# Kernel tuning notes

Measured on AMD Instinct MI355X. Metric: run time of the kernel, lower is better.

The kernel has to match this reference:

```python
import jax, jax.numpy as jnp
import numpy as np

EPS = 1e-6
GROUPS = 32


def group_norm(x, scale, bias):
    # x: [b, c, h, w], GroupNorm(32, c, eps=1e-6, affine=True)
    b, c, h, w = x.shape
    xg = x.reshape(b, GROUPS, c // GROUPS, h, w)
    mean = jnp.mean(xg, axis=(2, 3, 4), keepdims=True)
    var = jnp.var(xg, axis=(2, 3, 4), keepdims=True)
    xg = (xg - mean) * jax.lax.rsqrt(var + EPS)
    x = xg.reshape(b, c, h, w)
    return x * scale[None, :, None, None] + bias[None, :, None, None]


def conv1x1(x, w, b):
    # w: [out_c, in_c], b: [out_c]
    return jnp.einsum('oc,bchw->bohw', w, x) + b[None, :, None, None]


def setup_inputs() -> dict:
    key = jax.random.key(0)
    ks = jax.random.split(key, 12)
    c = 512
    b, h, w = 16, 32, 32
    s = 1.0 / np.sqrt(c)
    return {
        'x': jax.random.normal(ks[0], (b, c, h, w), jnp.float32),
        'y': jax.random.normal(ks[1], (b, c, h, w), jnp.float32),
        'norm_scale': jnp.ones((c,), jnp.float32),
        'norm_bias': jnp.zeros((c,), jnp.float32),
        'norm1_scale': jnp.ones((c,), jnp.float32),
        'norm1_bias': jnp.zeros((c,), jnp.float32),
        'wq': jax.random.normal(ks[2], (c, c), jnp.float32) * s,
        'bq': jnp.zeros((c,), jnp.float32),
        'wk': jax.random.normal(ks[3], (c, c), jnp.float32) * s,
        'bk': jnp.zeros((c,), jnp.float32),
        'wv': jax.random.normal(ks[4], (c, c), jnp.float32) * s,
        'bv': jnp.zeros((c,), jnp.float32),
        'wp': jax.random.normal(ks[5], (c, c), jnp.float32) * s,
        'bp': jnp.zeros((c,), jnp.float32),
    }


def reference(x, y, norm_scale, norm_bias, norm1_scale, norm1_bias,
              wq, bq, wk, bk, wv, bv, wp, bp):
    b, c, h, w = x.shape
    hw = h * w
    h_ = group_norm(x, norm_scale, norm_bias)
    k = conv1x1(h_, wk, bk).reshape(b, c, hw)          # [b, c, hw]
    v = conv1x1(h_, wv, bv).reshape(b, c, hw)          # [b, c, hw]
    y_ = group_norm(y, norm1_scale, norm1_bias)
    q = conv1x1(y_, wq, bq).reshape(b, c, hw)          # [b, c, hw]
    # attn[b, i, j] = sum_c q[b,c,i] * k[b,c,j]
    attn = jnp.einsum('bci,bcj->bij', q, k) * (int(c) ** -0.5)
    attn = jax.nn.softmax(attn, axis=2)
    # out[b, c, i] = sum_j v[b,c,j] * attn[b,i,j]
    out = jnp.einsum('bcj,bij->bci', v, attn).reshape(b, c, h, w)
    out = conv1x1(out, wp, bp)
    return x + out
```

## Files before the change

kernel.cpp:

```cpp
#include <hip/hip_runtime.h>
#include <hip/hip_bf16.h>

typedef __bf16 bf16;
typedef __bf16 bf16x8 __attribute__((ext_vector_type(8)));
typedef __bf16 bf16x4 __attribute__((ext_vector_type(4)));
typedef float f32x4 __attribute__((ext_vector_type(4)));
typedef unsigned short u16;
typedef unsigned short u16x8 __attribute__((ext_vector_type(8)));

constexpr int kHW = 1024;
constexpr int kC  = 512;

__device__ inline float wave_sum(float v) {
#pragma unroll
    for (int o = 32; o; o >>= 1) v += __shfl_xor(v, o, 64);
    return v;
}

__device__ inline float b2f(u16 u) {
    union { float f; unsigned i; } z; z.i = ((unsigned)u) << 16; return z.f;
}

__device__ inline void gload_lds16(const void* g, void* l) {
    __builtin_amdgcn_global_load_lds(
        (const __attribute__((address_space(1))) void*)g,
        (__attribute__((address_space(3))) void*)l, 16, 0, 0);
}

#define VMCNT(n) asm volatile("s_waitcnt vmcnt(" #n ")" ::: "memory")
#define SBAR __builtin_amdgcn_s_barrier()
#define NOP do {} while (0)

__global__ __launch_bounds__(256) void gn2w_kernel(
    const float* __restrict__ x0, const float* __restrict__ s0,
    const float* __restrict__ b0, bf16* __restrict__ o0,
    const float* __restrict__ x1, const float* __restrict__ s1,
    const float* __restrict__ b1, bf16* __restrict__ o1,
    const float* __restrict__ wq, const float* __restrict__ wk,
    const float* __restrict__ wv, const float* __restrict__ wp,
    const float* __restrict__ bq, const float* __restrict__ bk,
    const float* __restrict__ bv, const float* __restrict__ bp,
    bf16* __restrict__ wdst, float* __restrict__ bpk)
{
    int bid = blockIdx.x;
    int t = threadIdx.x;
    if (bid >= 1024) {
        int i = (bid - 1024) * 256 + t;
        wdst[i]            = (bf16)wq[i];
        wdst[262144 + i]   = (bf16)wk[i];
        wdst[2*262144 + i] = (bf16)wv[i];
        wdst[3*262144 + i] = (bf16)wp[i];
        if (i < 2048) {
            int j = i >> 9, c = i & 511;
            const float* s = j == 0 ? bq : j == 1 ? bk : j == 2 ? bv : bp;
            bpk[i] = s[c];
        }
        return;
    }

    __shared__ u16 xs[16][1032];
    __shared__ float red[8];
    __shared__ float ab[2][16];

    int xcd = bid & 7, idx = bid >> 3;
    int pair = xcd * 4 + (idx >> 5);
    int g = idx & 31;
    int sel = pair >> 4;
    int b = pair & 15;

    const float* x = sel ? x1 : x0;
    const float* scale = sel ? s1 : s0;
    const float* bias  = sel ? b1 : b0;
    bf16* outT = sel ? o1 : o0;

    int c0 = g * 16;
    const float* xg = x + ((size_t)b * kC + c0) * kHW;

    float s = 0.f, s2 = 0.f;
    const float4* xg4 = reinterpret_cast<const float4*>(xg);
#pragma unroll
    for (int i = 0; i < 16; ++i) {
        float4 v = xg4[t + i * 256];
        bf16x4 r;
        r[0] = (bf16)v.x; r[1] = (bf16)v.y; r[2] = (bf16)v.z; r[3] = (bf16)v.w;
        *reinterpret_cast<bf16x4*>(&xs[i][t * 4]) = r;
        s  += v.x + v.y + v.z + v.w;
        s2 += v.x*v.x + v.y*v.y + v.z*v.z + v.w*v.w;
    }
    s = wave_sum(s); s2 = wave_sum(s2);
    int lane = t & 63, wid = t >> 6;
    if (!lane) { red[wid] = s; red[4 + wid] = s2; }
    __syncthreads();
    float ts = red[0] + red[1] + red[2] + red[3];
    float t2 = red[4] + red[5] + red[6] + red[7];
    float mean = ts * (1.f / 16384.f);
    float var  = t2 * (1.f / 16384.f) - mean * mean;
    float inv  = rsqrtf(var + 1e-6f);

    if (t < 16) {
        float a = inv * scale[c0 + t];
        ab[0][t] = a;
        ab[1][t] = bias[c0 + t] - mean * a;
    }
    __syncthreads();

    int cg = t & 3, spw = t >> 2;
    float a0 = ab[0][cg*4],   a1 = ab[0][cg*4+1],
          a2 = ab[0][cg*4+2], a3 = ab[0][cg*4+3];
    float d0 = ab[1][cg*4],   d1 = ab[1][cg*4+1],
          d2 = ab[1][cg*4+2], d3 = ab[1][cg*4+3];
    bf16* ob = outT + (size_t)b * kHW * kC + c0 + cg * 4;
#pragma unroll
    for (int i = 0; i < 16; ++i) {
        int sp = spw + i * 64;
        bf16x4 w;
        w[0] = (bf16)(b2f(xs[cg*4 + 0][sp]) * a0 + d0);
        w[1] = (bf16)(b2f(xs[cg*4 + 1][sp]) * a1 + d1);
        w[2] = (bf16)(b2f(xs[cg*4 + 2][sp]) * a2 + d2);
        w[3] = (bf16)(b2f(xs[cg*4 + 3][sp]) * a3 + d3);
        *reinterpret_cast<bf16x4*>(ob + (size_t)sp * kC) = w;
    }
}

template <int BIAS, bool RESID, typename OUT_T, bool STATS, int NBX, int NBY>
__global__ __launch_bounds__(512, 2) void gemm256(
    const bf16* __restrict__ Ab, size_t sA, int lda,
    const bf16* __restrict__ Bb, size_t sB, int ldb,
    OUT_T* __restrict__ Cb, size_t sC, int ldc,
    const float* __restrict__ biasB, int sBias,
    const float* __restrict__ residB, size_t sR,
    float alpha, float* __restrict__ statsOut)
{
    __shared__ u16 lds[65536];
    constexpr int NT = 8;

    int bid = blockIdx.x, nwg = gridDim.x;
    int swz = (bid & 7) * (nwg >> 3) + (bid >> 3);
    int job = swz / (NBX * NBY), rem = swz % (NBX * NBY);
    int by = rem / NBX, bx = rem % NBX;
    int brow = by * 256, bcol = bx * 256;

    const u16* Au = reinterpret_cast<const u16*>(Ab + (size_t)job * sA);
    const u16* Bu = reinterpret_cast<const u16*>(Bb + (size_t)job * sB);

    int t = threadIdx.x;
    int lane = t & 63, w = t >> 6;
    int wm = w >> 2, wn = w & 3;
    int cc = lane & 15, nib = lane >> 4;

    int trow = t >> 3;
    int gsrc = ((t & 7) ^ (trow & 7)) * 8;
    const u16* Asrc = Au + (size_t)(brow + trow) * lda + gsrc;
    const u16* Bsrc = Bu + (size_t)(bcol + trow) * ldb + gsrc;
    u16* LDSA = lds;
    u16* LDSB = lds + 32768;

#define STAGE_A(TL, Q) gload_lds16(Asrc + (size_t)(Q) * 64 * lda + (TL) * 64, \
                                   LDSA + (((TL)&1)*4 + (Q)) * 4096 + t * 8)
#define STAGE_B(TL, Q) gload_lds16(Bsrc + (size_t)(Q) * 64 * ldb + (TL) * 64, \
                                   LDSB + (((TL)&1)*4 + (Q)) * 4096 + t * 8)

    f32x4 acc[8][4] = {};
    bf16x8 afr[4][2], bfr[4][2];

#define PHASE(MH, NH, TL, STG, WTC)                                           \
  {                                                                           \
    if ((NH) == 0) {                                                          \
      _Pragma("unroll") for (int mi = 0; mi < 4; ++mi)                        \
      _Pragma("unroll") for (int kx = 0; kx < 2; ++kx)                        \
        afr[mi][kx] = *reinterpret_cast<const bf16x8*>(LDSA +                 \
            (((TL)&1)*4 + wm*2 + (MH)) * 4096 + (mi*16 + cc) * 64 +           \
            (((nib + kx*4) ^ (cc & 7)) * 8));                                 \
    }                                                                         \
    if ((MH) == 0) {                                                          \
      _Pragma("unroll") for (int ni = 0; ni < 2; ++ni)                        \
      _Pragma("unroll") for (int kx = 0; kx < 2; ++kx)                        \
        bfr[(NH)*2 + ni][kx] = *reinterpret_cast<const bf16x8*>(LDSB +        \
            (((TL)&1)*4 + wn) * 4096 + (((NH)*2 + ni)*16 + cc) * 64 +         \
            (((nib + kx*4) ^ (cc & 7)) * 8));                                 \
    }                                                                         \
    STG;                                                                      \
    SBAR;                                                                     \
    __builtin_amdgcn_s_setprio(1);                                            \
    _Pragma("unroll") for (int mi = 0; mi < 4; ++mi)                          \
    _Pragma("unroll") for (int ni = 0; ni < 2; ++ni)                          \
    _Pragma("unroll") for (int kx = 0; kx < 2; ++kx)                          \
      acc[(MH)*4 + mi][(NH)*2 + ni] = __builtin_amdgcn_mfma_f32_16x16x32_bf16(\
          afr[mi][kx], bfr[(NH)*2 + ni][kx], acc[(MH)*4 + mi][(NH)*2 + ni],   \
          0, 0, 0);                                                           \
    __builtin_amdgcn_s_setprio(0);                                            \
    WTC;                                                                      \
    SBAR;                                                                     \
  }

    STAGE_A(0, 0); STAGE_A(0, 2); STAGE_B(0, 0); STAGE_B(0, 1);
    STAGE_B(0, 2); STAGE_B(0, 3); STAGE_A(0, 1); STAGE_A(0, 3);
    STAGE_A(1, 0); STAGE_A(1, 2); STAGE_B(1, 0); STAGE_B(1, 1);
    STAGE_B(1, 2); STAGE_B(1, 3); STAGE_A(1, 1); STAGE_A(1, 3);
    VMCNT(8);
    SBAR;

#pragma unroll
    for (int kt = 0; kt < NT; ++kt) {
        PHASE(0, 0, kt, NOP, NOP);
        PHASE(0, 1, kt,
              if (kt + 2 < NT) { STAGE_A(kt + 2, 0); STAGE_A(kt + 2, 2); },
              NOP);
        PHASE(1, 0, kt,
              if (kt + 2 < NT) { STAGE_B(kt + 2, 0); STAGE_B(kt + 2, 1); },
              NOP);
        PHASE(1, 1, kt,
              if (kt + 2 < NT) { STAGE_B(kt + 2, 2); STAGE_B(kt + 2, 3);
                                 STAGE_A(kt + 2, 1); STAGE_A(kt + 2, 3); },
              if (kt < NT - 2) { VMCNT(8); } else if (kt == NT - 2) { VMCNT(0); });
    }
#undef PHASE
#undef STAGE_A
#undef STAGE_B

#pragma unroll
    for (int m = 0; m < 8; ++m)
#pragma unroll
        for (int n = 0; n < 4; ++n)
#pragma unroll
            for (int r = 0; r < 4; ++r)
                acc[m][n][r] *= alpha;

    if constexpr (STATS) {
        float* sredS = reinterpret_cast<float*>(lds);
#pragma unroll
        for (int m = 0; m < 8; ++m)
#pragma unroll
            for (int r = 0; r < 4; ++r) {
                float s_ = 0.f;
#pragma unroll
                for (int n = 0; n < 4; ++n) {
                    float e = __expf(acc[m][n][r]);
                    acc[m][n][r] = e;
                    s_ += e;
                }
                s_ += __shfl_xor(s_, 1, 64);
                s_ += __shfl_xor(s_, 2, 64);
                s_ += __shfl_xor(s_, 4, 64);
                s_ += __shfl_xor(s_, 8, 64);
                if (cc == 0)
                    sredS[wn * 256 + wm * 128 + m * 16 + nib * 4 + r] = s_;
            }
        __syncthreads();
        if (t < 256) {
            float L = sredS[t] + sredS[256 + t] + sredS[512 + t] + sredS[768 + t];
            statsOut[((size_t)(job * 1024 + brow + t)) * 4 + bx] = L;
        }
    }

    OUT_T* Cj = Cb + (size_t)job * sC;
    const float* bias = biasB + (size_t)job * sBias;
#pragma unroll
    for (int m = 0; m < 8; ++m) {
#pragma unroll
        for (int n = 0; n < 4; ++n) {
#pragma unroll
            for (int r = 0; r < 4; ++r) {
                int grow = brow + wm * 128 + m * 16 + nib * 4 + r;
                int gcol = bcol + wn * 64 + n * 16 + cc;
                float vv = acc[m][n][r];
                if (BIAS == 1) vv += bias[grow];
                if (BIAS == 2) vv += bias[gcol];
                if (RESID)     vv += residB[(size_t)job * sR + (size_t)grow * ldc + gcol];
                Cj[(size_t)grow * ldc + gcol] = (OUT_T)vv;
            }
        }
    }
}

template <int BIAS, bool RESID, typename OUT_T, int NBX, int NBY, int NT, bool RSCALE>
__global__ __launch_bounds__(512, 4) void gemm128(
    const bf16* __restrict__ Ab, size_t sA, int lda,
    const bf16* __restrict__ Bb, size_t sB, int ldb,
    OUT_T* __restrict__ Cb, size_t sC, int ldc,
    const float* __restrict__ biasB, int sBias,
    const float* __restrict__ residB, size_t sR,
    const float* __restrict__ statsIn)
{
    __shared__ u16 lds[3 * 12288];

    int bid = blockIdx.x, nwg = gridDim.x;
    int swz = (bid & 7) * (nwg >> 3) + (bid >> 3);
    int job = swz / (NBX * NBY), rem = swz % (NBX * NBY);
    int by = rem / NBX, bx = rem % NBX;
    int brow = by * 128, bcol = bx * 256;

    const u16* Au = reinterpret_cast<const u16*>(Ab + (size_t)job * sA);
    const u16* Bu = reinterpret_cast<const u16*>(Bb + (size_t)job * sB);

    int t = threadIdx.x;
    int lane = t & 63, w = t >> 6;
    int wm = w >> 2, wn = w & 3;
    int cc = lane & 15, nib = lane >> 4;

    int trow = t >> 2;
    int gsrc = ((t & 3) ^ (trow & 3)) * 8;
    const u16* Asrc = Au + (size_t)(brow + trow) * lda + gsrc;
    const u16* Bsrc = Bu + (size_t)(bcol + trow) * ldb + gsrc;

#define STG_T(TL) {                                                           \
    u16* sl_ = lds + ((TL) % 3) * 12288;                                      \
    gload_lds16(Asrc + (TL) * 32,                       sl_ + t * 8);         \
    gload_lds16(Bsrc + (TL) * 32,                       sl_ + 4096 + t * 8);  \
    gload_lds16(Bsrc + (size_t)128 * ldb + (TL) * 32,   sl_ + 8192 + t * 8);  \
  }

    f32x4 acc[4][4] = {};
    int rsw = 0;

    STG_T(0); STG_T(1);
    VMCNT(3);
    SBAR;

#pragma unroll
    for (int kt = 0; kt < NT; ++kt) {
        if (kt + 2 < NT) STG_T(kt + 2);
        const u16* sb = lds + (kt % 3) * 12288;
        bf16x8 a[4], b[4];
#pragma unroll
        for (int mi = 0; mi < 4; ++mi)
            a[mi] = *reinterpret_cast<const bf16x8*>(sb +
                (wm * 64 + mi * 16 + cc) * 32 + ((nib ^ (cc & 3)) * 8));
#pragma unroll
        for (int ni = 0; ni < 4; ++ni)
            b[ni] = *reinterpret_cast<const bf16x8*>(sb + 4096 +
                (wn * 64 + ni * 16 + cc) * 32 + ((nib ^ (cc & 3)) * 8));
        __builtin_amdgcn_s_setprio(1);
#pragma unroll
        for (int mi = 0; mi < 4; ++mi)
#pragma unroll
            for (int ni = 0; ni < 4; ++ni)
                acc[mi][ni] = __builtin_amdgcn_mfma_f32_16x16x32_bf16(
                    a[mi], b[ni], acc[mi][ni], 0, 0, 0);
        __builtin_amdgcn_s_setprio(0);
        if (kt < NT - 2) { VMCNT(3); } else if (kt == NT - 2) { VMCNT(0); }
        SBAR;
    }
#undef STG_T
    (void)rsw;

    float* Ls = reinterpret_cast<float*>(lds);
    if constexpr (RSCALE) {
        __syncthreads();
        if (t < 128) {
            float4 sv = *reinterpret_cast<const float4*>(
                statsIn + ((size_t)(job * 1024 + brow + t)) * 4);
            Ls[t] = 1.0f / (sv.x + sv.y + sv.z + sv.w);
        }
        __syncthreads();
    }

    OUT_T* Cj = Cb + (size_t)job * sC;
    const float* bias = biasB + (size_t)job * sBias;
#pragma unroll
    for (int mi = 0; mi < 4; ++mi) {
#pragma unroll
        for (int ni = 0; ni < 4; ++ni) {
#pragma unroll
            for (int r = 0; r < 4; ++r) {
                int grow = brow + wm * 64 + mi * 16 + nib * 4 + r;
                int gcol = bcol + wn * 64 + ni * 16 + cc;
                float vv = acc[mi][ni][r];
                if constexpr (RSCALE) vv *= Ls[wm * 64 + mi * 16 + nib * 4 + r];
                if (BIAS == 1) vv += bias[grow];
                if (BIAS == 2) vv += bias[gcol];
                if (RESID)     vv += residB[(size_t)job * sR + (size_t)grow * ldc + gcol];
                Cj[(size_t)grow * ldc + gcol] = (OUT_T)vv;
            }
        }
    }
}

extern "C" void kernel_launch(void* const* d_in, const int* in_sizes, int n_in,
                              void* d_out, int out_size, void* d_ws, size_t ws_size,
                              hipStream_t stream)
{
    const float* x   = (const float*)d_in[0];
    const float* y   = (const float*)d_in[1];
    const float* ns  = (const float*)d_in[2];
    const float* nb  = (const float*)d_in[3];
    const float* n1s = (const float*)d_in[4];
    const float* n1b = (const float*)d_in[5];
    const float* wq  = (const float*)d_in[6];
    const float* bq  = (const float*)d_in[7];
    const float* wk  = (const float*)d_in[8];
    const float* bk  = (const float*)d_in[9];
    const float* wv  = (const float*)d_in[10];
    const float* bv  = (const float*)d_in[11];
    const float* wp  = (const float*)d_in[12];
    const float* bp  = (const float*)d_in[13];
    float* out = (float*)d_out;

    char* ws = (char*)d_ws;
    bf16* wbf  = (bf16*)ws;
    float* bpk = (float*)(ws + 2097152);
    bf16* ynT = (bf16*)(ws + 2105344);
    bf16* hnT = ynT + 8388608;
    bf16* qT  = hnT + 8388608;
    bf16* kT  = qT  + 8388608;
    bf16* v   = kT  + 8388608;
    float* stats = (float*)ynT;
    bf16* aoT = qT;
    bf16* P   = (bf16*)(ws + 2105344 + 5ull * 16777216);

    const size_t sBC = (size_t)kHW * kC;
    const float scl = 0.044194173824159216f;

    gn2w_kernel<<<2048, 256, 0, stream>>>(
        x, ns, nb, hnT, y, n1s, n1b, ynT,
        wq, wk, wv, wp, bq, bk, bv, bp, wbf, bpk);

    gemm256<2, false, bf16, false, 2, 64><<<256, 512, 0, stream>>>(
        ynT, 8388608, 512, wbf, 262144, 512, qT, 8388608, 512,
        bpk, 512, nullptr, 0, 1.f, nullptr);
    gemm128<1, false, bf16, 4, 4, 16, false><<<256, 512, 0, stream>>>(
        wbf + 2 * 262144, 0, 512, hnT, sBC, 512, v, sBC, 1024,
        bpk + 1024, 0, nullptr, 0, nullptr);
    gemm256<0, false, bf16, true, 4, 4><<<256, 512, 0, stream>>>(
        qT, sBC, 512, kT, sBC, 512, P, 1048576, 1024,
        bpk, 0, nullptr, 0, scl, stats);
    gemm128<0, false, bf16, 2, 8, 32, true><<<256, 512, 0, stream>>>(
        P, (size_t)1048576, 1024, v, sBC, 1024, aoT, sBC, 512,
        bpk, 0, nullptr, 0, stats);
    gemm128<1, true, float, 4, 4, 16, false><<<256, 512, 0, stream>>>(
        wbf + 3 * 262144, 0, 512, aoT, sBC, 512, out, sBC, 1024,
        bpk + 1536, 0, x, sBC, nullptr);
}
```

Measured before the change: 125.8 us.

## Restructure groupnorm kernel into 64-channel blocks with swizzled LDS and wide transposed stores

The fused groupnorm-plus-weight-cast kernel now uses 256 blocks of 512 threads, each handling 64 channels (four groups) of one image instead of one group per block. Rows are staged in LDS as bf16 with an XOR swizzle, then read back so each thread writes 16-byte bf16x8 chunks of the transposed [hw, c] output rather than 8-byte chunks. Weight and bias conversion is folded into every block instead of running in separate extra blocks. The trade-off is far fewer blocks (lower parallelism and latency hiding for a memory-bound pass) and about 132 KB of LDS per block, in exchange for wider, better-coalesced stores.

Measured after the change: 126.5 us. Within noise of the previous version (+0.6%).

```diff
diff --git a/kernel.cpp b/kernel.cpp
--- a/kernel.cpp
+++ b/kernel.cpp
@@ -4,6 +4,7 @@
 typedef __bf16 bf16;
 typedef __bf16 bf16x8 __attribute__((ext_vector_type(8)));
 typedef __bf16 bf16x4 __attribute__((ext_vector_type(4)));
+typedef __bf16 bf16x2 __attribute__((ext_vector_type(2)));
 typedef float f32x4 __attribute__((ext_vector_type(4)));
 typedef unsigned short u16;
 typedef unsigned short u16x8 __attribute__((ext_vector_type(8)));
@@ -31,7 +32,7 @@
 #define SBAR __builtin_amdgcn_s_barrier()
 #define NOP do {} while (0)
 
-__global__ __launch_bounds__(256) void gn2w_kernel(
+__global__ __launch_bounds__(512) void gn3_kernel(
     const float* __restrict__ x0, const float* __restrict__ s0,
     const float* __restrict__ b0, bf16* __restrict__ o0,
     const float* __restrict__ x1, const float* __restrict__ s1,
@@ -42,83 +43,107 @@
     const float* __restrict__ bv, const float* __restrict__ bp,
     bf16* __restrict__ wdst, float* __restrict__ bpk)
 {
+    __shared__ u16 xs[64 * 1032];
+    __shared__ float red[16];
+    __shared__ float ab[2][64];
+
     int bid = blockIdx.x;
     int t = threadIdx.x;
-    if (bid >= 1024) {
-        int i = (bid - 1024) * 256 + t;
-        wdst[i]            = (bf16)wq[i];
-        wdst[262144 + i]   = (bf16)wk[i];
-        wdst[2*262144 + i] = (bf16)wv[i];
-        wdst[3*262144 + i] = (bf16)wp[i];
-        if (i < 2048) {
-            int j = i >> 9, c = i & 511;
-            const float* s = j == 0 ? bq : j == 1 ? bk : j == 2 ? bv : bp;
-            bpk[i] = s[c];
-        }
-        return;
-    }
-
-    __shared__ u16 xs[16][1032];
-    __shared__ float red[8];
-    __shared__ float ab[2][16];
-
-    int xcd = bid & 7, idx = bid >> 3;
-    int pair = xcd * 4 + (idx >> 5);
-    int g = idx & 31;
-    int sel = pair >> 4;
-    int b = pair & 15;
+    int sel = bid >> 7, b = (bid >> 3) & 15, slice = bid & 7;
+    int c0 = slice * 64;
 
     const float* x = sel ? x1 : x0;
     const float* scale = sel ? s1 : s0;
     const float* bias  = sel ? b1 : b0;
     bf16* outT = sel ? o1 : o0;
 
-    int c0 = g * 16;
-    const float* xg = x + ((size_t)b * kC + c0) * kHW;
+    int row = t >> 3;
+    int cg8 = t & 7;
+    int wkey = (row >> 3) & 7;
+    const float* xr = x + ((size_t)b * kC + c0 + row) * kHW;
 
     float s = 0.f, s2 = 0.f;
-    const float4* xg4 = reinterpret_cast<const float4*>(xg);
-#pragma unroll
-    for (int i = 0; i < 16; ++i) {
-        float4 v = xg4[t + i * 256];
+#pragma unroll
+    for (int k = 0; k < 32; ++k) {
+        int colf4 = cg8 + 8 * k;
+        float4 v = reinterpret_cast<const float4*>(xr)[colf4];
+        int sp = colf4 * 4;
+        int g = sp >> 3;
+        int h = cg8 & 1;
+        int pg = g ^ wkey;
         bf16x4 r;
         r[0] = (bf16)v.x; r[1] = (bf16)v.y; r[2] = (bf16)v.z; r[3] = (bf16)v.w;
-        *reinterpret_cast<bf16x4*>(&xs[i][t * 4]) = r;
+        *reinterpret_cast<bf16x4*>(&xs[row * 1032 + pg * 8 + h * 4]) = r;
         s  += v.x + v.y + v.z + v.w;
         s2 += v.x*v.x + v.y*v.y + v.z*v.z + v.w*v.w;
     }
     s = wave_sum(s); s2 = wave_sum(s2);
-    int lane = t & 63, wid = t >> 6;
-    if (!lane) { red[wid] = s; red[4 + wid] = s2; }
+    int lane = t & 63, wvid = t >> 6;
+    if (!lane) { red[wvid * 2] = s; red[wvid * 2 + 1] = s2; }
     __syncthreads();
-    float ts = red[0] + red[1] + red[2] + red[3];
-    float t2 = red[4] + red[5] + red[6] + red[7];
-    float mean = ts * (1.f / 16384.f);
-    float var  = t2 * (1.f / 16384.f) - mean * mean;
-    float inv  = rsqrtf(var + 1e-6f);
-
-    if (t < 16) {
+    if (t < 64) {
+        int gi = t >> 4;
+        float ts = red[gi * 4]     + red[gi * 4 + 2];
+        float t2 = red[gi * 4 + 1] + red[gi * 4 + 3];
+        float mean = ts * (1.f / 16384.f);
+        float var  = t2 * (1.f / 16384.f) - mean * mean;
+        float inv  = rsqrtf(var + 1e-6f);
         float a = inv * scale[c0 + t];
         ab[0][t] = a;
         ab[1][t] = bias[c0 + t] - mean * a;
     }
     __syncthreads();
 
-    int cg = t & 3, spw = t >> 2;
-    float a0 = ab[0][cg*4],   a1 = ab[0][cg*4+1],
-          a2 = ab[0][cg*4+2], a3 = ab[0][cg*4+3];
-    float d0 = ab[1][cg*4],   d1 = ab[1][cg*4+1],
-          d2 = ab[1][cg*4+2], d3 = ab[1][cg*4+3];
-    bf16* ob = outT + (size_t)b * kHW * kC + c0 + cg * 4;
-#pragma unroll
-    for (int i = 0; i < 16; ++i) {
-        int sp = spw + i * 64;
-        bf16x4 w;
-        w[0] = (bf16)(b2f(xs[cg*4 + 0][sp]) * a0 + d0);
-        w[1] = (bf16)(b2f(xs[cg*4 + 1][sp]) * a1 + d1);
-        w[2] = (bf16)(b2f(xs[cg*4 + 2][sp]) * a2 + d2);
-        w[3] = (bf16)(b2f(xs[cg*4 + 3][sp]) * a3 + d3);
-        *reinterpret_cast<bf16x4*>(ob + (size_t)sp * kC) = w;
+    int c = t & 7;
+    int spblk = t >> 3;
+    float av[8], dv[8];
+#pragma unroll
+    for (int j = 0; j < 8; ++j) { av[j] = ab[0][c * 8 + j]; dv[j] = ab[1][c * 8 + j]; }
+    bf16* ob = outT + ((size_t)b * kHW) * kC + c0 + c * 8;
+#pragma unroll
+    for (int si = 0; si < 2; ++si) {
+        int g = spblk * 2 + si;
+        bf16x8 wsr[8];
+#pragma unroll
+        for (int j = 0; j < 8; ++j) {
+            int rrow = c * 8 + j;
+            int pg = g ^ c;
+            u16x8 vj = *reinterpret_cast<const u16x8*>(&xs[rrow * 1032 + pg * 8]);
+#pragma unroll
+            for (int e = 0; e < 8; ++e)
+                wsr[j][e] = (bf16)(b2f(vj[e]) * av[j] + dv[j]);
+        }
+        int sp0 = spblk * 16 + si * 8;
+#pragma unroll
+        for (int e = 0; e < 8; ++e) {
+            bf16x8 st;
+#pragma unroll
+            for (int j = 0; j < 8; ++j) st[j] = wsr[j][e];
+            *reinterpret_cast<bf16x8*>(ob + (size_t)(sp0 + e) * kC) = st;
+        }
+    }
+
+    {
+        int i = bid * 1024 + t * 2;
+        float2 vq = *reinterpret_cast<const float2*>(wq + i);
+        float2 vk = *reinterpret_cast<const float2*>(wk + i);
+        float2 vv = *reinterpret_cast<const float2*>(wv + i);
+        float2 vp = *reinterpret_cast<const float2*>(wp + i);
+        bf16x2 p;
+        p[0] = (bf16)vq.x; p[1] = (bf16)vq.y;
+        *reinterpret_cast<bf16x2*>(wdst + i) = p;
+        p[0] = (bf16)vk.x; p[1] = (bf16)vk.y;
+        *reinterpret_cast<bf16x2*>(wdst + 262144 + i) = p;
+        p[0] = (bf16)vv.x; p[1] = (bf16)vv.y;
+        *reinterpret_cast<bf16x2*>(wdst + 2 * 262144 + i) = p;
+        p[0] = (bf16)vp.x; p[1] = (bf16)vp.y;
+        *reinterpret_cast<bf16x2*>(wdst + 3 * 262144 + i) = p;
+        int ib = bid * 512 + t;
+        if (ib < 2048) {
+            int j = ib >> 9, cch = ib & 511;
+            const float* sb = j == 0 ? bq : j == 1 ? bk : j == 2 ? bv : bp;
+            bpk[ib] = sb[cch];
+        }
     }
 }
 
@@ -311,7 +336,6 @@
   }
 
     f32x4 acc[4][4] = {};
-    int rsw = 0;
 
     STG_T(0); STG_T(1);
     VMCNT(3);
@@ -342,7 +366,6 @@
         SBAR;
     }
 #undef STG_T
-    (void)rsw;
 
     float* Ls = reinterpret_cast<float*>(lds);
     if constexpr (RSCALE) {
@@ -411,7 +434,7 @@
     const size_t sBC = (size_t)kHW * kC;
     const float scl = 0.044194173824159216f;
 
-    gn2w_kernel<<<2048, 256, 0, stream>>>(
+    gn3_kernel<<<256, 512, 0, stream>>>(
         x, ns, nb, hnT, y, n1s, n1b, ynT,
         wq, wk, wv, wp, bq, bk, bv, bp, wbf, bpk);
 
```
